# Optimization experiments

Hardware: AMD Instinct MI355X
Metric: run time of the kernel (lower is better)

Reference implementation:

```python
import jax, jax.numpy as jnp
import numpy as np
from jax import lax

NUM_GROUP = 512    # G: number of FPS centers
GROUP_SIZE = 32    # M: KNN neighbors per center


def setup_inputs() -> dict:
    key = jax.random.key(0)
    xyz = jax.random.normal(key, (32, 8192, 3), dtype=jnp.float32)  # B N 3
    return {"xyz": xyz}


def _fps(xyz, num_group):
    """Iterative farthest point sampling. xyz: [B,N,3] -> idx [B,G] int32.
    Deterministic start at point 0 (matching pointnet2-style fps)."""
    B, N, _ = xyz.shape

    def step(carry, _):
        dists, last_idx = carry                       # dists: [B,N] running min sq-dist
        last = xyz[jnp.arange(B), last_idx]           # [B,3] most recent center
        d = jnp.sum((xyz - last[:, None, :]) ** 2, axis=-1)  # [B,N]
        dists = jnp.minimum(dists, d)
        nxt = jnp.argmax(dists, axis=-1).astype(jnp.int32)   # farthest point
        return (dists, nxt), nxt

    init_idx = jnp.zeros((B,), jnp.int32)
    init_d = jnp.full((B, N), jnp.inf, xyz.dtype)
    (_, _), idxs = lax.scan(step, (init_d, init_idx), None, length=num_group - 1)
    return jnp.concatenate([init_idx[None, :], idxs], axis=0).T  # [B,G]


def reference(xyz):
    B, N, _ = xyz.shape
    G, M = NUM_GROUP, GROUP_SIZE

    fps_idx = _fps(xyz, G)                              # [B,G] int32
    center = xyz[jnp.arange(B)[:, None], fps_idx]       # [B,G,3]

    # KNN: for each center, k nearest points in xyz (squared euclidean)
    # dist2[b,g,n] = |c|^2 + |x|^2 - 2 c.x   -> [B,G,N]
    x2 = jnp.sum(xyz * xyz, axis=-1)                    # [B,N]
    c2 = jnp.sum(center * center, axis=-1)              # [B,G]
    dist2 = c2[:, :, None] + x2[:, None, :] - 2.0 * jnp.einsum('bgd,bnd->bgn', center, xyz)
    _, idx = lax.top_k(-dist2, M)                       # [B,G,M] nearest-first

    neighborhood = xyz[jnp.arange(B)[:, None, None], idx]   # [B,G,M,3]
    neighborhood = neighborhood - center[:, :, None, :]
    return neighborhood, center, fps_idx
```

## Files before the change

### kernel.cpp

```cpp
#include <hip/hip_runtime.h>
#include <math.h>

#define BATCH  32
#define NPTS   8192
#define NGROUP 512
#define MSIZE  32

#define FPS_THREADS 512
#define SXYZ_FLOATS (NPTS * 3)
#define DYN_LDS_BYTES (SXYZ_FLOATS * 4)

typedef float  vf16 __attribute__((ext_vector_type(16)));
typedef unsigned int vu16 __attribute__((ext_vector_type(16)));

template<int CTRL>
__device__ __forceinline__ unsigned long long dpp_max_u64(unsigned long long k) {
    int lo2 = __builtin_amdgcn_update_dpp(0, (int)(unsigned)k,        CTRL, 0xF, 0xF, true);
    int hi2 = __builtin_amdgcn_update_dpp(0, (int)(unsigned)(k >> 32), CTRL, 0xF, 0xF, true);
    unsigned long long k2 = (((unsigned long long)(unsigned)hi2) << 32) | (unsigned)lo2;
    return k2 > k ? k2 : k;
}
template<int CTRL>
__device__ __forceinline__ unsigned long long dpp_min_u64(unsigned long long k) {
    int lo2 = __builtin_amdgcn_update_dpp(0, (int)(unsigned)k,        CTRL, 0xF, 0xF, true);
    int hi2 = __builtin_amdgcn_update_dpp(0, (int)(unsigned)(k >> 32), CTRL, 0xF, 0xF, true);
    unsigned long long k2 = (((unsigned long long)(unsigned)hi2) << 32) | (unsigned)lo2;
    return k2 < k ? k2 : k;
}

__global__ __launch_bounds__(FPS_THREADS, 2)
void fps_kernel(const float* __restrict__ xyz,
                float* __restrict__ out_center,
                float* __restrict__ out_fps)
{
#pragma clang fp contract(off)
    extern __shared__ float sxyz[];
    __shared__ unsigned long long partial[2][8];

    const int b    = blockIdx.x;
    const int t    = threadIdx.x;
    const int lane = t & 63;
    const int wid  = t >> 6;
    const float* bp = xyz + (size_t)b * NPTS * 3;
    const float4* bp4 = reinterpret_cast<const float4*>(bp);
    float4* s4 = reinterpret_cast<float4*>(sxyz);

    vf16 px, py, pz, dist;
    vu16 lo;
    #pragma unroll
    for (int c = 0; c < 4; ++c) {
        int f4 = c * 1536 + t * 3;
        float4 A = bp4[f4 + 0];
        float4 B = bp4[f4 + 1];
        float4 C = bp4[f4 + 2];
        s4[f4 + 0] = A; s4[f4 + 1] = B; s4[f4 + 2] = C;
        float xs[4] = {A.x, A.w, B.z, C.y};
        float ys[4] = {A.y, B.x, B.w, C.z};
        float zs[4] = {A.z, B.y, C.x, C.w};
        #pragma unroll
        for (int k = 0; k < 4; ++k) {
            int j = c * 4 + k;
            px[j] = xs[k]; py[j] = ys[k]; pz[j] = zs[k];
            dist[j] = INFINITY;
            lo[j] = ~(unsigned)(c * 2048 + t * 4 + k);
        }
    }
    __syncthreads();

    if (t == 0) {
        out_fps[(size_t)b * NGROUP] = 0.0f;
        out_center[(size_t)(b * NGROUP) * 3 + 0] = sxyz[0];
        out_center[(size_t)(b * NGROUP) * 3 + 1] = sxyz[1];
        out_center[(size_t)(b * NGROUP) * 3 + 2] = sxyz[2];
    }

    int last = 0;
    for (int g = 1; g < NGROUP; ++g) {
        const int p = g & 1;
        float lx = sxyz[last*3 + 0];
        float ly = sxyz[last*3 + 1];
        float lz = sxyz[last*3 + 2];

        unsigned long long kk[16];
        #pragma unroll
        for (int j = 0; j < 16; ++j) {
            float dx = px[j] - lx;
            float dy = py[j] - ly;
            float dz = pz[j] - lz;
            float d  = (dx*dx + dy*dy) + dz*dz;
            float nd = dist[j] < d ? dist[j] : d;
            dist[j] = nd;
            kk[j] = (((unsigned long long)__float_as_uint(nd)) << 32) | lo[j];
        }
        #pragma unroll
        for (int s = 8; s >= 1; s >>= 1) {
            #pragma unroll
            for (int i = 0; i < s; ++i)
                kk[i] = kk[i] >= kk[i+s] ? kk[i] : kk[i+s];
        }
        unsigned long long key = kk[0];
        key = dpp_max_u64<0xB1>(key);
        key = dpp_max_u64<0x4E>(key);
        key = dpp_max_u64<0x141>(key);
        key = dpp_max_u64<0x140>(key);
        key = dpp_max_u64<0x142>(key);
        key = dpp_max_u64<0x143>(key);
        if (lane == 63) partial[p][wid] = key;
        __syncthreads();
        unsigned long long fk = partial[p][0];
        #pragma unroll
        for (int w = 1; w < 8; ++w) {
            unsigned long long o = partial[p][w];
            if (o > fk) fk = o;
        }
        int fi = (int)(~(unsigned)fk);
        last = fi;
        if (t == 0) {
            out_fps[(size_t)b * NGROUP + g] = (float)fi;
            out_center[((size_t)(b * NGROUP + g)) * 3 + 0] = sxyz[fi*3 + 0];
            out_center[((size_t)(b * NGROUP + g)) * 3 + 1] = sxyz[fi*3 + 1];
            out_center[((size_t)(b * NGROUP + g)) * 3 + 2] = sxyz[fi*3 + 2];
        }
    }
}

__global__ __launch_bounds__(256)
void knn_kernel(const float* __restrict__ xyz,
                const float* __restrict__ center,
                float* __restrict__ out_nbhd)
{
    const int lane = threadIdx.x & 63;
    const int gid  = blockIdx.x * 4 + (threadIdx.x >> 6);
    const int b    = gid >> 9;
    const float* bp = xyz + (size_t)b * NPTS * 3;
    const float4* bp4 = reinterpret_cast<const float4*>(bp);

    const float cx = center[(size_t)gid*3+0];
    const float cy = center[(size_t)gid*3+1];
    const float cz = center[(size_t)gid*3+2];

    unsigned long long kl[4];
    #pragma unroll
    for (int k = 0; k < 4; ++k) kl[k] = ~0ULL;

    for (int c = 0; c < 32; ++c) {
        int f4 = c * 192 + lane * 3;
        float4 a  = bp4[f4+0];
        float4 bq = bp4[f4+1];
        float4 cq = bp4[f4+2];
        int p0 = c * 256 + lane * 4;
        float xs[4] = {a.x, a.w, bq.z, cq.y};
        float ys[4] = {a.y, bq.x, bq.w, cq.z};
        float zs[4] = {a.z, bq.y, cq.x, cq.w};
        #pragma unroll
        for (int k = 0; k < 4; ++k) {
            float dx = xs[k]-cx, dy = ys[k]-cy, dz = zs[k]-cz;
            float d = dx*dx + dy*dy + dz*dz;
            unsigned long long key =
                (((unsigned long long)__float_as_uint(d)) << 32) | (unsigned)(p0 + k);
            if (key < kl[3]) {
                kl[3] = key;
                #pragma unroll
                for (int q = 3; q > 0; --q) {
                    if (kl[q] < kl[q-1]) {
                        unsigned long long tk = kl[q]; kl[q] = kl[q-1]; kl[q-1] = tk;
                    }
                }
            }
        }
    }

    int keep = 0;
    #pragma unroll 1
    for (int r = 0; r < MSIZE; ++r) {
        unsigned long long k = kl[0];
        k = dpp_min_u64<0xB1>(k);
        k = dpp_min_u64<0x4E>(k);
        k = dpp_min_u64<0x141>(k);
        k = dpp_min_u64<0x140>(k);
        {
            unsigned long long o = __shfl_xor(k, 16);
            if (o < k) k = o;
            o = __shfl_xor(k, 32);
            if (o < k) k = o;
        }
        if (lane == r) keep = (int)(unsigned)k;
        if (kl[0] == k) {
            kl[0] = kl[1]; kl[1] = kl[2]; kl[2] = kl[3];
            kl[3] = ~0ULL;
        }
    }

    if (lane < MSIZE) {
        size_t o = ((size_t)gid * MSIZE + lane) * 3;
        float x = bp[keep*3+0], y = bp[keep*3+1], z = bp[keep*3+2];
        out_nbhd[o+0] = x - cx;
        out_nbhd[o+1] = y - cy;
        out_nbhd[o+2] = z - cz;
    }
}

extern "C" void kernel_launch(void* const* d_in, const int* in_sizes, int n_in,
                              void* d_out, int out_size, void* d_ws, size_t ws_size,
                              hipStream_t stream)
{
    const float* xyz = (const float*)d_in[0];
    float* out        = (float*)d_out;
    float* out_nbhd   = out;
    float* out_center = out + (size_t)BATCH*NGROUP*MSIZE*3;
    float* out_fps    = out_center + (size_t)BATCH*NGROUP*3;

    hipFuncSetAttribute(reinterpret_cast<const void*>(fps_kernel),
                        hipFuncAttributeMaxDynamicSharedMemorySize,
                        DYN_LDS_BYTES);

    fps_kernel<<<dim3(BATCH), dim3(FPS_THREADS), DYN_LDS_BYTES, stream>>>(xyz, out_center, out_fps);
    knn_kernel<<<dim3(BATCH*NGROUP/4), dim3(256), 0, stream>>>(xyz, out_center, out_nbhd);
}
```

Baseline: 685.5 us.

## Split FPS argmax into float max reduction then index-resolution pass

Replaces the packed 64-bit (distance, index) max reduction in the FPS loop with a 32-bit float max reduction across lanes and waves. Only waves whose local max equals the global max then run a second min-index reduction and resolve it via an LDS atomicMin. This halves the DPP work on the common path and drops the per-point index registers. In exchange it adds a second __syncthreads per iteration and a divergent branch.

Result: slower. 705.2 us (+2.9%).

```diff
diff --git a/kernel.cpp b/kernel.cpp
--- a/kernel.cpp
+++ b/kernel.cpp
@@ -10,15 +10,16 @@
 #define SXYZ_FLOATS (NPTS * 3)
 #define DYN_LDS_BYTES (SXYZ_FLOATS * 4)
 
-typedef float  vf16 __attribute__((ext_vector_type(16)));
-typedef unsigned int vu16 __attribute__((ext_vector_type(16)));
-
 template<int CTRL>
-__device__ __forceinline__ unsigned long long dpp_max_u64(unsigned long long k) {
-    int lo2 = __builtin_amdgcn_update_dpp(0, (int)(unsigned)k,        CTRL, 0xF, 0xF, true);
-    int hi2 = __builtin_amdgcn_update_dpp(0, (int)(unsigned)(k >> 32), CTRL, 0xF, 0xF, true);
-    unsigned long long k2 = (((unsigned long long)(unsigned)hi2) << 32) | (unsigned)lo2;
-    return k2 > k ? k2 : k;
+__device__ __forceinline__ float dpp_max_f32(float x) {
+    int o = __builtin_amdgcn_update_dpp(0, __float_as_int(x), CTRL, 0xF, 0xF, true);
+    float f = __int_as_float(o);
+    return x > f ? x : f;
+}
+template<int CTRL>
+__device__ __forceinline__ unsigned dpp_min_u32(unsigned x) {
+    unsigned o = (unsigned)__builtin_amdgcn_update_dpp(0, (int)x, CTRL, 0xF, 0xF, true);
+    return o < x ? o : x;
 }
 template<int CTRL>
 __device__ __forceinline__ unsigned long long dpp_min_u64(unsigned long long k) {
@@ -35,7 +36,8 @@
 {
 #pragma clang fp contract(off)
     extern __shared__ float sxyz[];
-    __shared__ unsigned long long partial[2][8];
+    __shared__ float        pmax[2][8];
+    __shared__ unsigned int sidx[2];
 
     const int b    = blockIdx.x;
     const int t    = threadIdx.x;
@@ -45,8 +47,7 @@
     const float4* bp4 = reinterpret_cast<const float4*>(bp);
     float4* s4 = reinterpret_cast<float4*>(sxyz);
 
-    vf16 px, py, pz, dist;
-    vu16 lo;
+    float px[16], py[16], pz[16], dist[16];
     #pragma unroll
     for (int c = 0; c < 4; ++c) {
         int f4 = c * 1536 + t * 3;
@@ -62,9 +63,9 @@
             int j = c * 4 + k;
             px[j] = xs[k]; py[j] = ys[k]; pz[j] = zs[k];
             dist[j] = INFINITY;
-            lo[j] = ~(unsigned)(c * 2048 + t * 4 + k);
-        }
-    }
+        }
+    }
+    if (t == 0) { sidx[0] = 0xFFFFFFFFu; sidx[1] = 0xFFFFFFFFu; }
     __syncthreads();
 
     if (t == 0) {
@@ -74,46 +75,66 @@
         out_center[(size_t)(b * NGROUP) * 3 + 2] = sxyz[2];
     }
 
+    const int tbase = t * 4;
     int last = 0;
     for (int g = 1; g < NGROUP; ++g) {
-        const int p = g & 1;
+        const int p = g & 1, q = p ^ 1;
         float lx = sxyz[last*3 + 0];
         float ly = sxyz[last*3 + 1];
         float lz = sxyz[last*3 + 2];
 
-        unsigned long long kk[16];
         #pragma unroll
         for (int j = 0; j < 16; ++j) {
             float dx = px[j] - lx;
             float dy = py[j] - ly;
             float dz = pz[j] - lz;
             float d  = (dx*dx + dy*dy) + dz*dz;
-            float nd = dist[j] < d ? dist[j] : d;
-            dist[j] = nd;
-            kk[j] = (((unsigned long long)__float_as_uint(nd)) << 32) | lo[j];
-        }
-        #pragma unroll
-        for (int s = 8; s >= 1; s >>= 1) {
+            dist[j] = dist[j] < d ? dist[j] : d;
+        }
+        float m01 = fmaxf(fmaxf(dist[0],  dist[1]),  fmaxf(dist[2],  dist[3]));
+        float m23 = fmaxf(fmaxf(dist[4],  dist[5]),  fmaxf(dist[6],  dist[7]));
+        float m45 = fmaxf(fmaxf(dist[8],  dist[9]),  fmaxf(dist[10], dist[11]));
+        float m67 = fmaxf(fmaxf(dist[12], dist[13]), fmaxf(dist[14], dist[15]));
+        float m = fmaxf(fmaxf(m01, m23), fmaxf(m45, m67));
+        m = dpp_max_f32<0xB1>(m);
+        m = dpp_max_f32<0x4E>(m);
+        m = dpp_max_f32<0x141>(m);
+        m = dpp_max_f32<0x140>(m);
+        m = dpp_max_f32<0x142>(m);
+        m = dpp_max_f32<0x143>(m);
+        float wmax = __int_as_float(__builtin_amdgcn_readlane(__float_as_int(m), 63));
+        if (lane == 63) pmax[p][wid] = wmax;
+        __syncthreads();
+
+        float gmax = fmaxf(
+            fmaxf(fmaxf(pmax[p][0], pmax[p][1]), fmaxf(pmax[p][2], pmax[p][3])),
+            fmaxf(fmaxf(pmax[p][4], pmax[p][5]), fmaxf(pmax[p][6], pmax[p][7])));
+        if (t == 0) sidx[q] = 0xFFFFFFFFu;
+
+        if (wmax == gmax) {
+            unsigned c0[16];
             #pragma unroll
-            for (int i = 0; i < s; ++i)
-                kk[i] = kk[i] >= kk[i+s] ? kk[i] : kk[i+s];
-        }
-        unsigned long long key = kk[0];
-        key = dpp_max_u64<0xB1>(key);
-        key = dpp_max_u64<0x4E>(key);
-        key = dpp_max_u64<0x141>(key);
-        key = dpp_max_u64<0x140>(key);
-        key = dpp_max_u64<0x142>(key);
-        key = dpp_max_u64<0x143>(key);
-        if (lane == 63) partial[p][wid] = key;
+            for (int j = 0; j < 16; ++j) {
+                unsigned gj = (unsigned)((j >> 2) * 2048 + tbase + (j & 3));
+                c0[j] = (dist[j] == gmax) ? gj : 0xFFFFFFFFu;
+            }
+            #pragma unroll
+            for (int s = 8; s >= 1; s >>= 1)
+                #pragma unroll
+                for (int i = 0; i < s; ++i)
+                    c0[i] = c0[i] < c0[i+s] ? c0[i] : c0[i+s];
+            unsigned mi = c0[0];
+            mi = dpp_min_u32<0xB1>(mi);
+            mi = dpp_min_u32<0x4E>(mi);
+            mi = dpp_min_u32<0x141>(mi);
+            mi = dpp_min_u32<0x140>(mi);
+            mi = dpp_min_u32<0x142>(mi);
+            mi = dpp_min_u32<0x143>(mi);
+            if (lane == 63) atomicMin(&sidx[p], mi);
+        }
         __syncthreads();
-        unsigned long long fk = partial[p][0];
-        #pragma unroll
-        for (int w = 1; w < 8; ++w) {
-            unsigned long long o = partial[p][w];
-            if (o > fk) fk = o;
-        }
-        int fi = (int)(~(unsigned)fk);
+
+        int fi = (int)sidx[p];
         last = fi;
         if (t == 0) {
             out_fps[(size_t)b * NGROUP + g] = (float)fi;
```
